# Kernel optimization log

Measured on AMD Instinct MI355X. Metric: run time of the kernel, lower is better.

## Reference

```python
import jax, jax.numpy as jnp
import numpy as np

N = 50000      # nodes
E = 800000     # edges (before self-loops)
IN = 128       # in_channels
HID = 16       # hidden_channels
HEADS = 8
OUT = 16       # out_channels
NEG_SLOPE = 0.2
BN_EPS = 1e-5
LN_EPS = 1e-5


def setup_inputs() -> dict:
    key = jax.random.key(0)
    ks = jax.random.split(key, 16)
    s = 0.05
    inp = {
        "x": jax.random.normal(ks[0], (N, IN), jnp.float32),
        "edge_index": jax.random.randint(ks[1], (2, E), 0, N, jnp.int64),
        # conv1 (in=IN, out=HID, heads=HEADS, concat=True)
        "Wl1": jax.random.normal(ks[2], (HEADS * HID, IN), jnp.float32) * s,
        "bl1": jnp.zeros((HEADS * HID,), jnp.float32),
        "Wr1": jax.random.normal(ks[3], (HEADS * HID, IN), jnp.float32) * s,
        "br1": jnp.zeros((HEADS * HID,), jnp.float32),
        "att1": jax.random.normal(ks[4], (HEADS, HID), jnp.float32) * s,
        "bias1": jnp.zeros((HEADS * HID,), jnp.float32),
        # batchnorm (eval mode, running stats)
        "bn_w": jnp.ones((HEADS * HID,), jnp.float32),
        "bn_b": jnp.zeros((HEADS * HID,), jnp.float32),
        "bn_rm": jnp.zeros((HEADS * HID,), jnp.float32),
        "bn_rv": jnp.ones((HEADS * HID,), jnp.float32),
        # conv2 (in=HEADS*HID, out=OUT, heads=HEADS, concat=False)
        "Wl2": jax.random.normal(ks[5], (HEADS * OUT, HEADS * HID), jnp.float32) * s,
        "bl2": jnp.zeros((HEADS * OUT,), jnp.float32),
        "Wr2": jax.random.normal(ks[6], (HEADS * OUT, HEADS * HID), jnp.float32) * s,
        "br2": jnp.zeros((HEADS * OUT,), jnp.float32),
        "att2": jax.random.normal(ks[7], (HEADS, OUT), jnp.float32) * s,
        "bias2": jnp.zeros((OUT,), jnp.float32),
        # skip + layernorm
        "Wskip": jax.random.normal(ks[8], (OUT, IN), jnp.float32) * s,
        "ln_w": jnp.ones((OUT,), jnp.float32),
        "ln_b": jnp.zeros((OUT,), jnp.float32),
    }
    return inp


def _gatv2(x, src, dst, Wl, bl, Wr, br, att, bias, heads, ch, concat):
    """PyG GATv2Conv (share_weights=False), eval mode (no dropout)."""
    n = x.shape[0]
    xl = (x @ Wl.T + bl).reshape(n, heads, ch)   # source transform
    xr = (x @ Wr.T + br).reshape(n, heads, ch)   # target transform
    # edge-wise attention score
    e = jax.nn.leaky_relu(xl[src] + xr[dst], NEG_SLOPE)          # [E',H,C]
    score = jnp.einsum('ehc,hc->eh', e, att)                      # [E',H]
    # segment softmax over incoming edges per destination node
    smax = jax.ops.segment_max(score, dst, num_segments=n)
    ex = jnp.exp(score - smax[dst])
    denom = jax.ops.segment_sum(ex, dst, num_segments=n)
    alpha = ex / denom[dst]                                       # [E',H]
    out = jax.ops.segment_sum(alpha[:, :, None] * xl[src], dst, num_segments=n)
    if concat:
        out = out.reshape(n, heads * ch)
    else:
        out = out.mean(axis=1)
    return out + bias


def reference(x, edge_index, Wl1, bl1, Wr1, br1, att1, bias1,
              bn_w, bn_b, bn_rm, bn_rv,
              Wl2, bl2, Wr2, br2, att2, bias2,
              Wskip, ln_w, ln_b):
    n = x.shape[0]
    loops = jnp.arange(n, dtype=edge_index.dtype)
    src = jnp.concatenate([edge_index[0], loops])
    dst = jnp.concatenate([edge_index[1], loops])

    x_res = x @ Wskip.T                                            # [N,OUT]

    h = _gatv2(x, src, dst, Wl1, bl1, Wr1, br1, att1, bias1, HEADS, HID, True)
    # BatchNorm1d in eval mode
    h = (h - bn_rm) * jax.lax.rsqrt(bn_rv + BN_EPS) * bn_w + bn_b
    h = jax.nn.elu(h)

    h = _gatv2(h, src, dst, Wl2, bl2, Wr2, br2, att2, bias2, HEADS, OUT, False)

    y = h + x_res
    mu = y.mean(axis=-1, keepdims=True)
    var = ((y - mu) ** 2).mean(axis=-1, keepdims=True)
    return (y - mu) * jax.lax.rsqrt(var + LN_EPS) * ln_w + ln_b
```

## Files before the change

### kernel.cpp

```cpp
#include <hip/hip_runtime.h>

#define NEG_SLOPE 0.2f
#define BN_EPS 1e-5f
#define LN_EPS 1e-5f

typedef __bf16 bf16_t;
typedef bf16_t bf16x8 __attribute__((ext_vector_type(8)));
typedef float floatx4 __attribute__((ext_vector_type(4)));

__device__ __forceinline__ unsigned short f2bf(float f) {
  unsigned u = __float_as_uint(f);
  u += 0x7FFFu + ((u >> 16) & 1u);
  return (unsigned short)(u >> 16);
}
__device__ __forceinline__ float bf_lo(unsigned u) { return __uint_as_float(u << 16); }
__device__ __forceinline__ float bf_hi(unsigned u) { return __uint_as_float(u & 0xFFFF0000u); }

__global__ void cvt_all(const float* __restrict__ x,
                        const float* __restrict__ wl1, const float* __restrict__ wr1,
                        const float* __restrict__ wl2, const float* __restrict__ wr2,
                        const float* __restrict__ wsk,
                        const float* __restrict__ bias1,
                        const float* __restrict__ bn_w, const float* __restrict__ bn_b,
                        const float* __restrict__ bn_rm, const float* __restrict__ bn_rv,
                        const int* __restrict__ ei, int E,
                        unsigned short* __restrict__ xbf,
                        unsigned short* __restrict__ wcat1,
                        unsigned short* __restrict__ wcat2,
                        int* __restrict__ deg, unsigned short* __restrict__ rpos,
                        float* __restrict__ bnS, float* __restrict__ bnT,
                        int n4x) {
  const int W4 = 128 * 128 / 4;
  const int S4 = 16 * 128 / 4;
  int i = blockIdx.x * blockDim.x + threadIdx.x;
  const float* src;
  unsigned short* dst;
  int j;
  if (i < n4x) { src = x; dst = xbf; j = i; }
  else {
    j = i - n4x;
    if (j < W4)               { src = wl1; dst = wcat1; }
    else if (j < 2 * W4)      { src = wr1; dst = wcat1 + 128 * 128; j -= W4; }
    else if (j < 3 * W4)      { src = wl2; dst = wcat2; j -= 2 * W4; }
    else if (j < 4 * W4)      { src = wr2; dst = wcat2 + 128 * 128; j -= 3 * W4; }
    else if (j < 4 * W4 + S4) { src = wsk; dst = wcat1 + 256 * 128; j -= 4 * W4; }
    else {
      j -= 4 * W4 + S4;
      if (j < 32) {
        for (int t = j * 4; t < j * 4 + 4; ++t) {
          float S = bn_w[t] * rsqrtf(bn_rv[t] + BN_EPS);
          bnS[t] = S;
          bnT[t] = (bias1[t] - bn_rm[t]) * S + bn_b[t];
        }
      } else {
        int e = j - 32;
        if (e < E) {
          int d = ei[E + e];
          rpos[e] = (unsigned short)atomicAdd(&deg[d], 1);
        }
      }
      return;
    }
  }
  float4 v = ((const float4*)src)[j];
  ushort4 o;
  o.x = f2bf(v.x); o.y = f2bf(v.y); o.z = f2bf(v.z); o.w = f2bf(v.w);
  ((ushort4*)dst)[j] = o;
}

__global__ __launch_bounds__(1024)
void scan_deg(const int* __restrict__ deg, int* __restrict__ indptr, int n) {
  __shared__ int carry;
  __shared__ int wsum[16];
  int lane = threadIdx.x & 63, wid = threadIdx.x >> 6;
  if (threadIdx.x == 0) { carry = 0; indptr[0] = 0; }
  __syncthreads();
  for (int base = 0; base < n; base += 4096) {
    int i0 = base + (int)threadIdx.x * 4;
    int4 v = make_int4(0, 0, 0, 0);
    if (i0 + 3 < n) v = *(const int4*)(deg + i0);
    else {
      if (i0 < n)     v.x = deg[i0];
      if (i0 + 1 < n) v.y = deg[i0 + 1];
      if (i0 + 2 < n) v.z = deg[i0 + 2];
      if (i0 + 3 < n) v.w = deg[i0 + 3];
    }
    int s1 = v.x, s2 = s1 + v.y, s3 = s2 + v.z, s4 = s3 + v.w;
    int s = s4;
#pragma unroll
    for (int d = 1; d < 64; d <<= 1) { int t = __shfl_up(s, d, 64); if (lane >= d) s += t; }
    if (lane == 63) wsum[wid] = s;
    __syncthreads();
    if (threadIdx.x < 16) {
      int ws = wsum[threadIdx.x];
#pragma unroll
      for (int d = 1; d < 16; d <<= 1) { int t = __shfl_up(ws, d, 16); if ((int)threadIdx.x >= d) ws += t; }
      wsum[threadIdx.x] = ws;
    }
    __syncthreads();
    int off = carry + (wid ? wsum[wid - 1] : 0) + (s - s4);
    if (i0 < n)     indptr[i0 + 1] = off + s1;
    if (i0 + 1 < n) indptr[i0 + 2] = off + s2;
    if (i0 + 2 < n) indptr[i0 + 3] = off + s3;
    if (i0 + 3 < n) indptr[i0 + 4] = off + s4;
    __syncthreads();
    if (threadIdx.x == 0) carry += wsum[15];
    __syncthreads();
  }
}

__global__ void scatter_edges(const int* __restrict__ ei, int E,
                              const int* __restrict__ indptr,
                              const unsigned short* __restrict__ rpos,
                              unsigned short* __restrict__ csr) {
  int e = blockIdx.x * blockDim.x + threadIdx.x;
  if (e < E) {
    int d = ei[E + e];
    csr[indptr[d] + (int)rpos[e]] = (unsigned short)ei[e];
  }
}

template <bool MIXED>
__global__ __launch_bounds__(256)
void gemm_bf16_mfma(const unsigned short* __restrict__ A, const unsigned short* __restrict__ B,
                    const float* __restrict__ bias0, const float* __restrict__ bias1,
                    unsigned short* __restrict__ Cbf, float* __restrict__ Cf,
                    int M, int pstrips) {
  int wave = (int)((blockIdx.x * blockDim.x + threadIdx.x) >> 6);
  int lane = threadIdx.x & 63;
  int mtiles = (M + 31) >> 5;
  if (wave >= mtiles * pstrips) return;
  int mt = wave % mtiles, ps = wave / mtiles;
  int r = lane & 15, quad = lane >> 4;

  const unsigned short* Abase = A + (size_t)(mt * 32 + r) * 128 + quad * 8;
  bf16x8 a0[4], a1[4];
#pragma unroll
  for (int k = 0; k < 4; ++k) {
    a0[k] = *(const bf16x8*)(Abase + 32 * k);
    a1[k] = *(const bf16x8*)(Abase + 16 * 128 + 32 * k);
  }

  int row0 = mt * 32 + quad * 4;
  const int Ptot = MIXED ? 272 : 256;
#pragma unroll
  for (int pp = 0; pp < 4; ++pp) {
    int p0 = ps * 64 + pp * 16;
    if (p0 >= Ptot) break;
    const unsigned short* Bbase = B + (size_t)(p0 + r) * 128 + quad * 8;
    bf16x8 b[4];
#pragma unroll
    for (int k = 0; k < 4; ++k) b[k] = *(const bf16x8*)(Bbase + 32 * k);
    floatx4 acc0 = {0.f, 0.f, 0.f, 0.f};
    floatx4 acc1 = {0.f, 0.f, 0.f, 0.f};
#pragma unroll
    for (int k = 0; k < 4; ++k) {
      acc0 = __builtin_amdgcn_mfma_f32_16x16x32_bf16(a0[k], b[k], acc0, 0, 0, 0);
      acc1 = __builtin_amdgcn_mfma_f32_16x16x32_bf16(a1[k], b[k], acc1, 0, 0, 0);
    }
    int col = p0 + r;
    if (MIXED && col >= 256) {
#pragma unroll
      for (int i = 0; i < 4; ++i) {
        if (row0 + i < M)      Cf[(size_t)(row0 + i) * 16 + (col - 256)] = acc0[i];
        if (row0 + 16 + i < M) Cf[(size_t)(row0 + 16 + i) * 16 + (col - 256)] = acc1[i];
      }
    } else {
      float bs = (col < 128) ? bias0[col] : bias1[col - 128];
#pragma unroll
      for (int i = 0; i < 4; ++i) {
        if (row0 + i < M)      Cbf[(size_t)(row0 + i) * 256 + col] = f2bf(acc0[i] + bs);
        if (row0 + 16 + i < M) Cbf[(size_t)(row0 + 16 + i) * 256 + col] = f2bf(acc1[i] + bs);
      }
    }
  }
}

template <int LAYER>
__global__ __launch_bounds__(256)
void gat_agg(const unsigned int* __restrict__ xlr,
             const int* __restrict__ indptr, const unsigned short* __restrict__ csr,
             const float* __restrict__ att,
             const float* __restrict__ p0, const float* __restrict__ p1,
             const float* __restrict__ p2, const float* __restrict__ p3,
             void* __restrict__ outp, int n, int nwaves) {
  int lane = threadIdx.x & 63;
  int gw = (int)((blockIdx.x * blockDim.x + threadIdx.x) >> 6);
  int half = lane >> 5, sl = lane & 31;
  float4 at = ((const float4*)att)[sl];
  float a0 = 0.6f * at.x, a1 = 0.6f * at.y, a2 = 0.6f * at.z, a3 = 0.6f * at.w;

  for (int dst = gw; dst < n; dst += nwaves) {
    int beg = indptr[dst], end = indptr[dst + 1];
    int tot = end - beg + 1;
    uint2 ur = *(const uint2*)(xlr + (size_t)dst * 128 + 64 + sl * 2);
    float xr0 = bf_lo(ur.x), xr1 = bf_hi(ur.x), xr2 = bf_lo(ur.y), xr3 = bf_hi(ur.y);
    float lA = 0.f, lB = 0.f;
    float cA0 = 0.f, cA1 = 0.f, cA2 = 0.f, cA3 = 0.f;
    float cB0 = 0.f, cB1 = 0.f, cB2 = 0.f, cB3 = 0.f;
    for (int base = 0; base < tot; base += 64) {
      int g = beg + base + lane;
      int myidx = (g < end) ? (int)csr[g] : dst;
      int items = min(64, tot - base);
      for (int j = 0; j < items; j += 4) {
        int s0 = __shfl(myidx, j + half);
        int s1 = __shfl(myidx, j + 2 + half);
        uint2 u0 = *(const uint2*)(xlr + (size_t)s0 * 128 + sl * 2);
        uint2 u1 = *(const uint2*)(xlr + (size_t)s1 * 128 + sl * 2);
        float vmA = (j + half < items) ? 1.f : 0.f;
        float vmB = (j + 2 + half < items) ? 1.f : 0.f;
        {
          float x0 = bf_lo(u0.x), x1 = bf_hi(u0.x), x2 = bf_lo(u0.y), x3 = bf_hi(u0.y);
          float e0 = x0 + xr0, e1 = x1 + xr1, e2 = x2 + xr2, e3 = x3 + xr3;
          float sc =            fmaf(fmaf(fabsf(e0), 0.66666667f, e0), a0,
                                fmaf(fmaf(fabsf(e1), 0.66666667f, e1), a1,
                                fmaf(fmaf(fabsf(e2), 0.66666667f, e2), a2,
                                     fmaf(fabsf(e3), 0.66666667f, e3) * a3)));
          sc += __shfl_xor(sc, 1);
          sc += __shfl_xor(sc, 2);
          float p = __expf(sc) * vmA;
          lA += p;
          cA0 = fmaf(p, x0, cA0); cA1 = fmaf(p, x1, cA1);
          cA2 = fmaf(p, x2, cA2); cA3 = fmaf(p, x3, cA3);
        }
        {
          float x0 = bf_lo(u1.x), x1 = bf_hi(u1.x), x2 = bf_lo(u1.y), x3 = bf_hi(u1.y);
          float e0 = x0 + xr0, e1 = x1 + xr1, e2 = x2 + xr2, e3 = x3 + xr3;
          float sc =            fmaf(fmaf(fabsf(e0), 0.66666667f, e0), a0,
                                fmaf(fmaf(fabsf(e1), 0.66666667f, e1), a1,
                                fmaf(fmaf(fabsf(e2), 0.66666667f, e2), a2,
                                     fmaf(fabsf(e3), 0.66666667f, e3) * a3)));
          sc += __shfl_xor(sc, 1);
          sc += __shfl_xor(sc, 2);
          float p = __expf(sc) * vmB;
          lB += p;
          cB0 = fmaf(p, x0, cB0); cB1 = fmaf(p, x1, cB1);
          cB2 = fmaf(p, x2, cB2); cB3 = fmaf(p, x3, cB3);
        }
      }
    }
    float l = lA + lB;
    float c0 = cA0 + cB0, c1 = cA1 + cB1, c2 = cA2 + cB2, c3 = cA3 + cB3;
    l  += __shfl_xor(l, 32);
    c0 += __shfl_xor(c0, 32); c1 += __shfl_xor(c1, 32);
    c2 += __shfl_xor(c2, 32); c3 += __shfl_xor(c3, 32);
    float inv = 1.f / l;

    if (LAYER == 1) {
      float4 S = ((const float4*)p0)[sl];
      float4 T = ((const float4*)p1)[sl];
      float o0 = fmaf(c0 * inv, S.x, T.x);
      float o1 = fmaf(c1 * inv, S.y, T.y);
      float o2 = fmaf(c2 * inv, S.z, T.z);
      float o3 = fmaf(c3 * inv, S.w, T.w);
      o0 = (o0 > 0.f) ? o0 : (__expf(o0) - 1.f);
      o1 = (o1 > 0.f) ? o1 : (__expf(o1) - 1.f);
      o2 = (o2 > 0.f) ? o2 : (__expf(o2) - 1.f);
      o3 = (o3 > 0.f) ? o3 : (__expf(o3) - 1.f);
      if (half == 0) {
        uint2 o;
        o.x = ((unsigned)f2bf(o1) << 16) | f2bf(o0);
        o.y = ((unsigned)f2bf(o3) << 16) | f2bf(o2);
        ((uint2*)outp)[(size_t)dst * 32 + sl] = o;
      }
    } else {
      float y0 = c0 * inv, y1 = c1 * inv, y2 = c2 * inv, y3 = c3 * inv;
#pragma unroll
      for (int d = 4; d <= 16; d <<= 1) {
        y0 += __shfl_xor(y0, d); y1 += __shfl_xor(y1, d);
        y2 += __shfl_xor(y2, d); y3 += __shfl_xor(y3, d);
      }
      int chh = (sl & 3) * 4;
      float4 b2 = *(const float4*)(p1 + chh);
      float4 xs = *(const float4*)(p0 + (size_t)dst * 16 + chh);
      y0 = y0 * 0.125f + b2.x + xs.x;
      y1 = y1 * 0.125f + b2.y + xs.y;
      y2 = y2 * 0.125f + b2.z + xs.z;
      y3 = y3 * 0.125f + b2.w + xs.w;
      float t = (y0 + y1) + (y2 + y3);
      t += __shfl_xor(t, 1); t += __shfl_xor(t, 2);
      float mu = t * (1.f / 16.f);
      float d0 = y0 - mu, d1 = y1 - mu, d2 = y2 - mu, d3 = y3 - mu;
      float v = (d0 * d0 + d1 * d1) + (d2 * d2 + d3 * d3);
      v += __shfl_xor(v, 1); v += __shfl_xor(v, 2);
      float istd = rsqrtf(v * (1.f / 16.f) + LN_EPS);
      float4 lw = *(const float4*)(p2 + chh);
      float4 lb = *(const float4*)(p3 + chh);
      if (lane < 4) {
        float4 o;
        o.x = d0 * istd * lw.x + lb.x;
        o.y = d1 * istd * lw.y + lb.y;
        o.z = d2 * istd * lw.z + lb.z;
        o.w = d3 * istd * lw.w + lb.w;
        *(float4*)((float*)outp + (size_t)dst * 16 + chh) = o;
      }
    }
  }
}

extern "C" void kernel_launch(void* const* d_in, const int* in_sizes, int n_in,
                              void* d_out, int out_size, void* d_ws, size_t ws_size,
                              hipStream_t stream) {
  const float* x     = (const float*)d_in[0];
  const int*   ei    = (const int*)d_in[1];
  const float* Wl1   = (const float*)d_in[2];
  const float* bl1   = (const float*)d_in[3];
  const float* Wr1   = (const float*)d_in[4];
  const float* br1   = (const float*)d_in[5];
  const float* att1  = (const float*)d_in[6];
  const float* bias1 = (const float*)d_in[7];
  const float* bn_w  = (const float*)d_in[8];
  const float* bn_b  = (const float*)d_in[9];
  const float* bn_rm = (const float*)d_in[10];
  const float* bn_rv = (const float*)d_in[11];
  const float* Wl2   = (const float*)d_in[12];
  const float* bl2   = (const float*)d_in[13];
  const float* Wr2   = (const float*)d_in[14];
  const float* br2   = (const float*)d_in[15];
  const float* att2  = (const float*)d_in[16];
  const float* bias2 = (const float*)d_in[17];
  const float* Wskip = (const float*)d_in[18];
  const float* ln_w  = (const float*)d_in[19];
  const float* ln_b  = (const float*)d_in[20];

  const int N = in_sizes[0] / 128;
  const int E = in_sizes[1] / 2;

  char* w = (char*)d_ws;
  size_t off = 0;
  auto alloc = [&](size_t bytes) -> void* {
    void* p = (void*)(w + off);
    off += (bytes + 255) & ~(size_t)255;
    return p;
  };
  unsigned short* xbf    = (unsigned short*)alloc((size_t)N * 128 * 2);
  unsigned short* wcat1  = (unsigned short*)alloc(272 * 128 * 2);
  unsigned short* wcat2  = (unsigned short*)alloc(256 * 128 * 2);
  unsigned int*   xlr    = (unsigned int*)alloc((size_t)N * 128 * 4);
  float*          xres   = (float*)alloc((size_t)N * 16 * 4);
  unsigned short* hbf    = (unsigned short*)alloc((size_t)N * 128 * 2);
  float*          bnS    = (float*)alloc(128 * 4);
  float*          bnT    = (float*)alloc(128 * 4);
  int*            deg    = (int*)alloc((size_t)N * 4);
  int*            indptr = (int*)alloc((size_t)(N + 1) * 4);
  unsigned short* rpos   = (unsigned short*)alloc((size_t)E * 2);
  unsigned short* csr    = (unsigned short*)alloc((size_t)E * 2);

  hipMemsetAsync(deg, 0, (size_t)N * 4, stream);
  {
    int n4x = (N * 128) / 4;
    int tot = n4x + 4 * (128 * 128 / 4) + (16 * 128 / 4) + 32 + E;
    cvt_all<<<(tot + 255) / 256, 256, 0, stream>>>(
        x, Wl1, Wr1, Wl2, Wr2, Wskip, bias1, bn_w, bn_b, bn_rm, bn_rv, ei, E,
        xbf, wcat1, wcat2, deg, rpos, bnS, bnT, n4x);
  }

  scan_deg<<<1, 1024, 0, stream>>>(deg, indptr, N);
  scatter_edges<<<(E + 255) / 256, 256, 0, stream>>>(ei, E, indptr, rpos, csr);

  {
    int mtiles = (N + 31) >> 5;
    int waves = mtiles * 5;
    gemm_bf16_mfma<true><<<(waves + 3) / 4, 256, 0, stream>>>(
        xbf, wcat1, bl1, br1, (unsigned short*)xlr, xres, N, 5);
  }

  {
    int blocks = 2048, nwaves = blocks * 4;
    gat_agg<1><<<blocks, 256, 0, stream>>>(xlr, indptr, csr, att1,
                                           bnS, bnT, nullptr, nullptr, (void*)hbf, N, nwaves);
  }

  {
    int mtiles = (N + 31) >> 5;
    int waves = mtiles * 4;
    gemm_bf16_mfma<false><<<(waves + 3) / 4, 256, 0, stream>>>(
        hbf, wcat2, bl2, br2, (unsigned short*)xlr, nullptr, N, 4);
  }

  {
    int blocks = 2048, nwaves = blocks * 4;
    gat_agg<2><<<blocks, 256, 0, stream>>>(xlr, indptr, csr, att2,
                                           xres, bias2, ln_w, ln_b, d_out, N, nwaves);
  }
}
```

Before: 334.1 us.

## Pad CSR rows to even length and load neighbor indices as packed pairs

The degree scan now rounds each row length up to an even count, so every CSR row starts 4-byte aligned. The aggregation kernel then reads neighbor index pairs as 32-bit words directly in each lane, replacing the wave-wide load and shuffle broadcast. It also unrolls four pairs per step so eight gathers are in flight, and uses readfirstlane to make the per-row metadata scalar. The CSR buffer grows to hold the padding, and reads can run past a row's end, though those entries are masked out.

```diff
diff --git a/kernel.cpp b/kernel.cpp
--- a/kernel.cpp
+++ b/kernel.cpp
@@ -85,6 +85,7 @@
       if (i0 + 2 < n) v.z = deg[i0 + 2];
       if (i0 + 3 < n) v.w = deg[i0 + 3];
     }
+    v.x = (v.x + 1) & ~1; v.y = (v.y + 1) & ~1; v.z = (v.z + 1) & ~1; v.w = (v.w + 1) & ~1;
     int s1 = v.x, s2 = s1 + v.y, s3 = s2 + v.z, s4 = s3 + v.w;
     int s = s4;
 #pragma unroll
@@ -179,7 +180,8 @@
 template <int LAYER>
 __global__ __launch_bounds__(256)
 void gat_agg(const unsigned int* __restrict__ xlr,
-             const int* __restrict__ indptr, const unsigned short* __restrict__ csr,
+             const int* __restrict__ indptr, const int* __restrict__ deg,
+             const unsigned short* __restrict__ csr,
              const float* __restrict__ att,
              const float* __restrict__ p0, const float* __restrict__ p1,
              const float* __restrict__ p2, const float* __restrict__ p3,
@@ -191,51 +193,53 @@
   float a0 = 0.6f * at.x, a1 = 0.6f * at.y, a2 = 0.6f * at.z, a3 = 0.6f * at.w;
 
   for (int dst = gw; dst < n; dst += nwaves) {
-    int beg = indptr[dst], end = indptr[dst + 1];
-    int tot = end - beg + 1;
-    uint2 ur = *(const uint2*)(xlr + (size_t)dst * 128 + 64 + sl * 2);
+    int dsts = __builtin_amdgcn_readfirstlane(dst);
+    int beg = __builtin_amdgcn_readfirstlane(indptr[dsts]);
+    int dg = __builtin_amdgcn_readfirstlane(deg[dsts]);
+    const unsigned* cp = (const unsigned*)csr + (beg >> 1);
+    int tot = dg + 1;
+    int npair = (tot + 1) >> 1;
+
+    uint2 ur = *(const uint2*)(xlr + (size_t)dsts * 128 + 64 + sl * 2);
     float xr0 = bf_lo(ur.x), xr1 = bf_hi(ur.x), xr2 = bf_lo(ur.y), xr3 = bf_hi(ur.y);
     float lA = 0.f, lB = 0.f;
     float cA0 = 0.f, cA1 = 0.f, cA2 = 0.f, cA3 = 0.f;
     float cB0 = 0.f, cB1 = 0.f, cB2 = 0.f, cB3 = 0.f;
-    for (int base = 0; base < tot; base += 64) {
-      int g = beg + base + lane;
-      int myidx = (g < end) ? (int)csr[g] : dst;
-      int items = min(64, tot - base);
-      for (int j = 0; j < items; j += 4) {
-        int s0 = __shfl(myidx, j + half);
-        int s1 = __shfl(myidx, j + 2 + half);
-        uint2 u0 = *(const uint2*)(xlr + (size_t)s0 * 128 + sl * 2);
-        uint2 u1 = *(const uint2*)(xlr + (size_t)s1 * 128 + sl * 2);
-        float vmA = (j + half < items) ? 1.f : 0.f;
-        float vmB = (j + 2 + half < items) ? 1.f : 0.f;
-        {
-          float x0 = bf_lo(u0.x), x1 = bf_hi(u0.x), x2 = bf_lo(u0.y), x3 = bf_hi(u0.y);
-          float e0 = x0 + xr0, e1 = x1 + xr1, e2 = x2 + xr2, e3 = x3 + xr3;
-          float sc =            fmaf(fmaf(fabsf(e0), 0.66666667f, e0), a0,
-                                fmaf(fmaf(fabsf(e1), 0.66666667f, e1), a1,
-                                fmaf(fmaf(fabsf(e2), 0.66666667f, e2), a2,
-                                     fmaf(fabsf(e3), 0.66666667f, e3) * a3)));
-          sc += __shfl_xor(sc, 1);
-          sc += __shfl_xor(sc, 2);
-          float p = __expf(sc) * vmA;
-          lA += p;
-          cA0 = fmaf(p, x0, cA0); cA1 = fmaf(p, x1, cA1);
-          cA2 = fmaf(p, x2, cA2); cA3 = fmaf(p, x3, cA3);
-        }
-        {
-          float x0 = bf_lo(u1.x), x1 = bf_hi(u1.x), x2 = bf_lo(u1.y), x3 = bf_hi(u1.y);
-          float e0 = x0 + xr0, e1 = x1 + xr1, e2 = x2 + xr2, e3 = x3 + xr3;
-          float sc =            fmaf(fmaf(fabsf(e0), 0.66666667f, e0), a0,
-                                fmaf(fmaf(fabsf(e1), 0.66666667f, e1), a1,
-                                fmaf(fmaf(fabsf(e2), 0.66666667f, e2), a2,
-                                     fmaf(fabsf(e3), 0.66666667f, e3) * a3)));
-          sc += __shfl_xor(sc, 1);
-          sc += __shfl_xor(sc, 2);
-          float p = __expf(sc) * vmB;
-          lB += p;
-          cB0 = fmaf(p, x0, cB0); cB1 = fmaf(p, x1, cB1);
-          cB2 = fmaf(p, x2, cB2); cB3 = fmaf(p, x3, cB3);
+
+    for (int p = 0; p < npair; p += 4) {
+      uint2 u[4];
+      float vm[4];
+#pragma unroll
+      for (int k = 0; k < 4; ++k) {
+        unsigned pr = cp[p + k];
+        int e0 = 2 * (p + k), e1 = e0 + 1;
+        int sA = (e0 < dg) ? (int)(pr & 0xFFFFu) : dsts;
+        int sB = (e1 < dg) ? (int)(pr >> 16) : dsts;
+        float mA = (e0 < tot) ? 1.f : 0.f;
+        float mB = (e1 < tot) ? 1.f : 0.f;
+        int s = half ? sB : sA;
+        vm[k] = half ? mB : mA;
+        u[k] = *(const uint2*)(xlr + ((size_t)s << 7) + sl * 2);
+      }
+#pragma unroll
+      for (int k = 0; k < 4; ++k) {
+        float x0 = bf_lo(u[k].x), x1 = bf_hi(u[k].x), x2 = bf_lo(u[k].y), x3 = bf_hi(u[k].y);
+        float e0 = x0 + xr0, e1 = x1 + xr1, e2 = x2 + xr2, e3 = x3 + xr3;
+        float sc = fmaf(fmaf(fabsf(e0), 0.66666667f, e0), a0,
+                   fmaf(fmaf(fabsf(e1), 0.66666667f, e1), a1,
+                   fmaf(fmaf(fabsf(e2), 0.66666667f, e2), a2,
+                        fmaf(fabsf(e3), 0.66666667f, e3) * a3)));
+        sc += __shfl_xor(sc, 1);
+        sc += __shfl_xor(sc, 2);
+        float pw = __expf(sc) * vm[k];
+        if (k & 1) {
+          lB += pw;
+          cB0 = fmaf(pw, x0, cB0); cB1 = fmaf(pw, x1, cB1);
+          cB2 = fmaf(pw, x2, cB2); cB3 = fmaf(pw, x3, cB3);
+        } else {
+          lA += pw;
+          cA0 = fmaf(pw, x0, cA0); cA1 = fmaf(pw, x1, cA1);
+          cA2 = fmaf(pw, x2, cA2); cA3 = fmaf(pw, x3, cA3);
         }
       }
     }
@@ -344,7 +348,7 @@
   int*            deg    = (int*)alloc((size_t)N * 4);
   int*            indptr = (int*)alloc((size_t)(N + 1) * 4);
   unsigned short* rpos   = (unsigned short*)alloc((size_t)E * 2);
-  unsigned short* csr    = (unsigned short*)alloc((size_t)E * 2);
+  unsigned short* csr    = (unsigned short*)alloc((size_t)(E + N) * 2 + 256);
 
   hipMemsetAsync(deg, 0, (size_t)N * 4, stream);
   {
@@ -367,7 +371,7 @@
 
   {
     int blocks = 2048, nwaves = blocks * 4;
-    gat_agg<1><<<blocks, 256, 0, stream>>>(xlr, indptr, csr, att1,
+    gat_agg<1><<<blocks, 256, 0, stream>>>(xlr, indptr, deg, csr, att1,
                                            bnS, bnT, nullptr, nullptr, (void*)hbf, N, nwaves);
   }
 
@@ -380,7 +384,7 @@
 
   {
     int blocks = 2048, nwaves = blocks * 4;
-    gat_agg<2><<<blocks, 256, 0, stream>>>(xlr, indptr, csr, att2,
+    gat_agg<2><<<blocks, 256, 0, stream>>>(xlr, indptr, deg, csr, att2,
                                            xres, bias2, ln_w, ln_b, d_out, N, nwaves);
   }
 }
```

New measurement: 323.7 us. 1.03x faster.
